# Kernel tuning notes

Measured on AMD Instinct MI355X. Metric: run time of the kernel, lower is better.

Reference implementation:

```python
import jax, jax.numpy as jnp
import numpy as np

B, S, D, H, DH = 2, 1024, 1024, 16, 64  # batch, seq, dim_model, heads, dim_head


def setup_inputs() -> dict:
    key = jax.random.key(0)
    ks = jax.random.split(key, 9)
    def W(k):
        return jax.random.normal(k, (D, D), jnp.float32) * 0.02
    z = jnp.zeros((D,), jnp.float32)
    return {
        "x": jax.random.normal(ks[0], (B, S, D), jnp.float32),
        "rel_pos_emb": jax.random.normal(ks[1], (B, S, D), jnp.float32),
        "padding_mask": jnp.zeros((B, S), jnp.int32),
        "Wq": W(ks[2]), "bq": z,
        "Wk": W(ks[3]), "bk": z,
        "Wv": W(ks[4]), "bv": z,
        "Wqr": W(ks[5]), "bqr": z,
        "Wkr": W(ks[6]), "bkr": z,
        "Wc": W(ks[7]), "bc": z,
    }


def reference(x, rel_pos_emb, padding_mask, Wq, bq, Wk, bk, Wv, bv, Wqr, bqr, Wkr, bkr, Wc, bc):
    b, s, d = x.shape

    def proj(t, W_, b_):  # (b,s,D) -> (b,H,s,DH)
        return (t @ W_.T + b_).reshape(b, s, H, DH).transpose(0, 2, 1, 3)

    q = proj(x, Wq, bq)
    k = proj(x, Wk, bk)
    v = proj(x, Wv, bv)
    qr = proj(rel_pos_emb, Wqr, bqr)
    kr = proj(rel_pos_emb, Wkr, bkr)

    # relative position index: clamp(i - j + MAX_REL_POS/2, 0, MAX_REL_POS-1), MAX_REL_POS = S
    idx = jnp.arange(s)
    pos = jnp.clip(idx[:, None] - idx[None, :] + s // 2, 0, s - 1)  # (s,s) int
    pos_b = jnp.broadcast_to(pos[None, None], (b, H, s, s))

    c2c = jnp.einsum('bhid,bhjd->bhij', q, k)
    c2p_att = jnp.einsum('bhid,bhjd->bhij', q, kr)
    c2p = jnp.take_along_axis(c2p_att, pos_b, axis=-1)   # gather along last dim
    p2c_att = jnp.einsum('bhid,bhjd->bhij', qr, k)
    p2c = jnp.take_along_axis(p2c_att, pos_b, axis=-2)   # gather along query dim

    scale = jnp.sqrt(jnp.asarray(3 * DH, jnp.float32))
    scores = (c2c + c2p + p2c) / scale
    scores = jnp.where(padding_mask[:, None, None, :] == 1, -jnp.inf, scores)
    attn = jax.nn.softmax(scores, axis=-1)  # dropout is identity in eval

    out = jnp.einsum('bhij,bhjd->bhid', attn, v)
    out = out.transpose(0, 2, 1, 3).reshape(b, s, H * DH)
    return out @ Wc.T + bc
```

## Files before the change

kernel.cpp:

```cpp
#include <hip/hip_runtime.h>

typedef unsigned short u16;
typedef unsigned int   u32;
typedef __bf16 bf16x8 __attribute__((ext_vector_type(8)));
typedef float  f32x4  __attribute__((ext_vector_type(4)));

__device__ __forceinline__ float b2f(u16 s) { return __uint_as_float(((u32)s) << 16); }
__device__ __forceinline__ u16 f2b(float f) {
  u32 x = __float_as_uint(f);
  return (u16)((x + 0x7FFFu + ((x >> 16) & 1u)) >> 16);
}

#if __has_builtin(__builtin_amdgcn_exp2f)
#define EXP2(x) __builtin_amdgcn_exp2f(x)
#else
#define EXP2(x) exp2f(x)
#endif

template <int C>
__device__ __forceinline__ u32 dppu(u32 s) {
  return (u32)__builtin_amdgcn_update_dpp((int)s, (int)s, C, 0xF, 0xF, false);
}
__device__ __forceinline__ float red_sum16(float x) {
  x += __uint_as_float(dppu<0x128>(__float_as_uint(x)));
  x += __uint_as_float(dppu<0x124>(__float_as_uint(x)));
  x += __uint_as_float(dppu<0x122>(__float_as_uint(x)));
  x += __uint_as_float(dppu<0x121>(__float_as_uint(x)));
  return x;
}

union U16x8 { uint4 u; u16 s[8]; };

__device__ __forceinline__ uint4 cvt8(const float4 a, const float4 b) {
  U16x8 r;
  r.s[0] = f2b(a.x); r.s[1] = f2b(a.y); r.s[2] = f2b(a.z); r.s[3] = f2b(a.w);
  r.s[4] = f2b(b.x); r.s[5] = f2b(b.y); r.s[6] = f2b(b.z); r.s[7] = f2b(b.w);
  return r.u;
}

typedef __attribute__((address_space(3))) u32 lds_u32;
typedef const __attribute__((address_space(1))) u32 glb_u32;
__device__ __forceinline__ void gld16(const u16* gp, u16* lp) {
  __builtin_amdgcn_global_load_lds((glb_u32*)gp, (lds_u32*)lp, 16, 0, 0);
}

struct CvtArgs { const float* s[8]; u16* d[8]; int n[8]; };

__global__ __launch_bounds__(256) void cvt_bf16(CvtArgs c) {
  const int t = blockIdx.y;
  const int i = (blockIdx.x * 256 + threadIdx.x) * 8;
  if (i >= c.n[t]) return;
  const float4 a = *(const float4*)(c.s[t] + i);
  const float4 b = *(const float4*)(c.s[t] + i + 4);
  *(uint4*)(c.d[t] + i) = cvt8(a, b);
}

struct GemmBArgs { const u16* A[5]; const u16* W[5]; const float* Bi[5]; void* C[5]; int vtz; };

template <int BM, int BN, bool OUT_F32>
__global__ __launch_bounds__(256) void gemm_lds(GemmBArgs g, int M, int N, int K) {
  const int z = blockIdx.z;
  const u16* __restrict__ A = g.A[z];
  const u16* __restrict__ W = g.W[z];
  const float* __restrict__ Bi = g.Bi[z];

  const int m0 = blockIdx.y * BM, n0 = blockIdx.x * BN;
  const int tid = threadIdx.x, wv = tid >> 6, lane = tid & 63;
  const int wm = wv >> 1, wn = wv & 1;
  const int lr = lane & 15, lq = lane >> 4;
  constexpr int MT = BM / 32;
  constexpr int NT = BN / 32;

  __shared__ u16 As[BM * 64];
  __shared__ u16 Ws[BN * 64];

  const f32x4 vzero = {0.f, 0.f, 0.f, 0.f};
  f32x4 acc[MT][NT];
#pragma unroll
  for (int i = 0; i < MT; ++i)
#pragma unroll
    for (int j = 0; j < NT; ++j) acc[i][j] = vzero;

  const int srow = lane >> 3;
  const int sc   = (lane & 7) ^ srow;

  for (int kb = 0; kb < K; kb += 64) {
    __syncthreads();
#pragma unroll
    for (int t = 0; t < MT; ++t) {
      const u16* gp = A + (size_t)(m0 + t * 32 + wv * 8 + srow) * K + kb + sc * 8;
      gld16(gp, As + (t * 32 + wv * 8) * 64 + lane * 8);
    }
#pragma unroll
    for (int t = 0; t < NT; ++t) {
      const u16* gp = W + (size_t)(n0 + t * 32 + wv * 8 + srow) * K + kb + sc * 8;
      gld16(gp, Ws + (t * 32 + wv * 8) * 64 + lane * 8);
    }
    __syncthreads();
#pragma unroll
    for (int kk = 0; kk < 2; ++kk) {
      bf16x8 af[MT], bw[NT];
#pragma unroll
      for (int mt = 0; mt < MT; ++mt) {
        const int row = wm * (BM / 2) + mt * 16 + lr;
        af[mt] = *(const bf16x8*)&As[row * 64 + (((kk << 2) | lq) ^ (row & 7)) * 8];
      }
#pragma unroll
      for (int nt = 0; nt < NT; ++nt) {
        const int row = wn * (BN / 2) + nt * 16 + lr;
        bw[nt] = *(const bf16x8*)&Ws[row * 64 + (((kk << 2) | lq) ^ (row & 7)) * 8];
      }
#pragma unroll
      for (int mt = 0; mt < MT; ++mt)
#pragma unroll
        for (int nt = 0; nt < NT; ++nt)
          acc[mt][nt] = __builtin_amdgcn_mfma_f32_16x16x32_bf16(af[mt], bw[nt], acc[mt][nt], 0, 0, 0);
    }
  }

#pragma unroll
  for (int mt = 0; mt < MT; ++mt) {
#pragma unroll
    for (int nt = 0; nt < NT; ++nt) {
      const int col = n0 + wn * (BN / 2) + nt * 16 + lr;
      const float bia = Bi[col];
      const int row0 = m0 + wm * (BM / 2) + mt * 16 + lq * 4;
      if (OUT_F32) {
#pragma unroll
        for (int r = 0; r < 4; ++r)
          ((float*)g.C[z])[(size_t)(row0 + r) * N + col] = acc[mt][nt][r] + bia;
      } else if (z == g.vtz) {
        ushort4 pk;
        pk.x = f2b(acc[mt][nt][0] + bia); pk.y = f2b(acc[mt][nt][1] + bia);
        pk.z = f2b(acc[mt][nt][2] + bia); pk.w = f2b(acc[mt][nt][3] + bia);
        const int bb = row0 >> 10, s0 = row0 & 1023;
        *(ushort4*)((u16*)g.C[z] + ((size_t)bb << 20) + ((size_t)col << 10) + s0) = pk;
      } else {
#pragma unroll
        for (int r = 0; r < 4; ++r)
          ((u16*)g.C[z])[(size_t)(row0 + r) * N + col] = f2b(acc[mt][nt][r] + bia);
      }
    }
  }
}

struct GemmArgs { const void* A[5]; const float* W[5]; const float* Bi[5]; void* C[5]; int vtz; };

template <bool A_F32, bool OUT_F32>
__global__ __launch_bounds__(256) void gemm5(GemmArgs g, int M, int N, int K) {
  const int z = blockIdx.z;
  const float* __restrict__ Wf = g.W[z];
  const float* __restrict__ Bi = g.Bi[z];

  const int m0 = blockIdx.y * 128, n0 = blockIdx.x * 128;
  const int tid = threadIdx.x;
  const int wv = tid >> 6, lane = tid & 63;
  const int wm = wv >> 1, wn = wv & 1;
  const int lr = lane & 15, lq = lane >> 4;

  __shared__ alignas(16) u16 As[128][64];
  __shared__ alignas(16) u16 Ws[128][64];

  const f32x4 vzero = {0.f, 0.f, 0.f, 0.f};
  f32x4 acc[4][4];
#pragma unroll
  for (int i = 0; i < 4; ++i)
#pragma unroll
    for (int j = 0; j < 4; ++j) acc[i][j] = vzero;

  const int srow = tid >> 1;
  const int sc0  = (tid & 1) * 32;
  const float* pw = Wf + (size_t)(n0 + srow) * K + sc0;
  const float* paf = A_F32 ? ((const float*)g.A[z] + (size_t)(m0 + srow) * K + sc0) : nullptr;
  const u16*   pab = A_F32 ? nullptr : ((const u16*)g.A[z] + (size_t)(m0 + srow) * K + sc0);

  for (int k0 = 0; k0 < K; k0 += 64) {
#pragma unroll
    for (int u_ = 0; u_ < 4; ++u_) {
      const float4 w0 = *(const float4*)(pw + k0 + u_ * 8);
      const float4 w1 = *(const float4*)(pw + k0 + u_ * 8 + 4);
      *(uint4*)&Ws[srow][sc0 + u_ * 8] = cvt8(w0, w1);
      if (A_F32) {
        const float4 a0 = *(const float4*)(paf + k0 + u_ * 8);
        const float4 a1 = *(const float4*)(paf + k0 + u_ * 8 + 4);
        *(uint4*)&As[srow][sc0 + u_ * 8] = cvt8(a0, a1);
      } else {
        *(uint4*)&As[srow][sc0 + u_ * 8] = *(const uint4*)(pab + k0 + u_ * 8);
      }
    }
    __syncthreads();
#pragma unroll
    for (int kk = 0; kk < 2; ++kk) {
      bf16x8 af[4], bfr[4];
#pragma unroll
      for (int mt = 0; mt < 4; ++mt)
        af[mt] = *(const bf16x8*)&As[wm * 64 + mt * 16 + lr][kk * 32 + lq * 8];
#pragma unroll
      for (int nt = 0; nt < 4; ++nt)
        bfr[nt] = *(const bf16x8*)&Ws[wn * 64 + nt * 16 + lr][kk * 32 + lq * 8];
#pragma unroll
      for (int mt = 0; mt < 4; ++mt)
#pragma unroll
        for (int nt = 0; nt < 4; ++nt)
          acc[mt][nt] = __builtin_amdgcn_mfma_f32_16x16x32_bf16(af[mt], bfr[nt], acc[mt][nt], 0, 0, 0);
    }
    __syncthreads();
  }

#pragma unroll
  for (int mt = 0; mt < 4; ++mt) {
#pragma unroll
    for (int nt = 0; nt < 4; ++nt) {
      const int col = n0 + wn * 64 + nt * 16 + lr;
      const float bia = Bi[col];
      const int row0 = m0 + wm * 64 + mt * 16 + lq * 4;
      if (OUT_F32) {
#pragma unroll
        for (int r = 0; r < 4; ++r)
          ((float*)g.C[z])[(size_t)(row0 + r) * N + col] = acc[mt][nt][r] + bia;
      } else if (z == g.vtz) {
        ushort4 pk;
        pk.x = f2b(acc[mt][nt][0] + bia); pk.y = f2b(acc[mt][nt][1] + bia);
        pk.z = f2b(acc[mt][nt][2] + bia); pk.w = f2b(acc[mt][nt][3] + bia);
        const int bb = row0 >> 10, s0 = row0 & 1023;
        *(ushort4*)((u16*)g.C[z] + ((size_t)bb << 20) + ((size_t)col << 10) + s0) = pk;
      } else {
#pragma unroll
        for (int r = 0; r < 4; ++r)
          ((u16*)g.C[z])[(size_t)(row0 + r) * N + col] = f2b(acc[mt][nt][r] + bia);
      }
    }
  }
}

__global__ __launch_bounds__(256, 2) void attn_wave(
    const u16* __restrict__ q, const u16* __restrict__ k,
    const u16* __restrict__ vT, const u16* __restrict__ qr,
    const u16* __restrict__ kr, const int* __restrict__ pmask,
    u16* __restrict__ ao) {
  constexpr int S = 1024, Dm = 1024;
  constexpr int GP = 37;
  constexpr int PBP = 74;
  constexpr int WLDS = 9472;

  __shared__ alignas(16) char smem[4 * WLDS];

  const int bx = blockIdx.x;
  const int bh = bx & 31, it = bx >> 5;
  const int bb = bh >> 4, h = bh & 15;
  const int i0 = it * 32;

  const int tid = threadIdx.x;
  const int wv = tid >> 6, lane = tid & 63;
  const int lq = lane >> 4, lr = lane & 15;

  char* wbase = smem + wv * WLDS;
  float* G1f = (float*)wbase;
  float* G2f = (float*)(wbase + 4736);
  u16*   Pb  = (u16*)wbase;

  const u16* qb  = q  + ((size_t)bb << 20) + h * 64;
  const u16* kb  = k  + ((size_t)bb << 20) + h * 64;
  const u16* qrb = qr + ((size_t)bb << 20) + h * 64;
  const u16* krb = kr + ((size_t)bb << 20) + h * 64;
  const u16* vtb = vT + ((size_t)bb << 20) + ((size_t)h << 16);
  const int* pmb = pmask + ((size_t)bb << 10);

  const float kscale = 1.44269504088896f / 13.856406460551018f;

  bf16x8 qf[2][2];
#pragma unroll
  for (int mt = 0; mt < 2; ++mt)
#pragma unroll
    for (int kk = 0; kk < 2; ++kk)
      qf[mt][kk] = *(const bf16x8*)(qb + (size_t)(i0 + mt * 16 + lr) * Dm + kk * 32 + lq * 8);

  const f32x4 vzero = {0.f, 0.f, 0.f, 0.f};
  f32x4 o[2][4];
#pragma unroll
  for (int mt = 0; mt < 2; ++mt)
#pragma unroll
    for (int nd = 0; nd < 4; ++nd) o[mt][nd] = vzero;
  float lst[2][4];
#pragma unroll
  for (int mt = 0; mt < 2; ++mt)
#pragma unroll
    for (int r = 0; r < 4; ++r) lst[mt][r] = 0.f;

#pragma unroll 1
  for (int t8 = 0; t8 < 8; ++t8) {
    const int j0 = (wv + t8 * 4) * 32;
    const int pb_ = i0 - j0 + 481;

    bf16x8 kf[2][2];
#pragma unroll
    for (int nt = 0; nt < 2; ++nt) {
      const u16* kp = kb + (size_t)(j0 + nt * 16 + lr) * Dm + lq * 8;
      kf[nt][0] = *(const bf16x8*)kp;
      kf[nt][1] = *(const bf16x8*)(kp + 32);
    }
    const int mv0 = pmb[j0 + lr], mv1 = pmb[j0 + 16 + lr];

    f32x4 cc[2][2];
#pragma unroll
    for (int mt = 0; mt < 2; ++mt)
#pragma unroll
      for (int nt = 0; nt < 2; ++nt) {
        f32x4 a = vzero;
        a = __builtin_amdgcn_mfma_f32_16x16x32_bf16(qf[mt][0], kf[nt][0], a, 0, 0, 0);
        a = __builtin_amdgcn_mfma_f32_16x16x32_bf16(qf[mt][1], kf[nt][1], a, 0, 0, 0);
        cc[mt][nt] = a;
      }

#pragma unroll
    for (int n4 = 0; n4 < 4; ++n4) {
      int p = pb_ + n4 * 16 + lr;
      p = p < 0 ? 0 : (p > 1023 ? 1023 : p);
      const u16* kp = krb + (size_t)p * Dm + lq * 8;
      const u16* qp = qrb + (size_t)p * Dm + lq * 8;
      const bf16x8 kr0 = *(const bf16x8*)kp;
      const bf16x8 kr1 = *(const bf16x8*)(kp + 32);
      const bf16x8 qr0 = *(const bf16x8*)qp;
      const bf16x8 qr1 = *(const bf16x8*)(qp + 32);
      const int tb = n4 * 16 + lr;
#pragma unroll
      for (int mt = 0; mt < 2; ++mt) {
        f32x4 a = vzero;
        a = __builtin_amdgcn_mfma_f32_16x16x32_bf16(qf[mt][0], kr0, a, 0, 0, 0);
        a = __builtin_amdgcn_mfma_f32_16x16x32_bf16(qf[mt][1], kr1, a, 0, 0, 0);
#pragma unroll
        for (int r = 0; r < 4; ++r) {
          const int arow = mt * 16 + lq * 4 + r;
          int u = tb - arow;
          u = u < -2 ? -2 : (u > 34 ? 34 : u);
          G1f[2 + arow * GP + u] = a[r];
        }
      }
#pragma unroll
      for (int mt = 0; mt < 2; ++mt) {
        f32x4 g = vzero;
        g = __builtin_amdgcn_mfma_f32_16x16x32_bf16(kf[mt][0], qr0, g, 0, 0, 0);
        g = __builtin_amdgcn_mfma_f32_16x16x32_bf16(kf[mt][1], qr1, g, 0, 0, 0);
#pragma unroll
        for (int r = 0; r < 4; ++r) {
          const int brow = mt * 16 + lq * 4 + r;
          int u = tb + brow - 31;
          u = u < -2 ? -2 : (u > 34 ? 34 : u);
          G2f[2 + brow * GP + u] = g[r];
        }
      }
    }

    u32 pk[2][4];
#pragma unroll
    for (int mt = 0; mt < 2; ++mt) {
#pragma unroll
      for (int r = 0; r < 4; ++r) {
        const int a_ = mt * 16 + lq * 4 + r;
        float s0 = cc[mt][0][r] + G1f[2 + a_ * GP + 31 - lr] + G2f[2 + lr * GP + a_];
        float s1 = cc[mt][1][r] + G1f[2 + a_ * GP + 15 - lr] + G2f[2 + (16 + lr) * GP + a_];
        s0 = mv0 ? -1e30f : s0 * kscale;
        s1 = mv1 ? -1e30f : s1 * kscale;
        const float p0 = EXP2(s0);
        const float p1 = EXP2(s1);
        lst[mt][r] += p0 + p1;
        pk[mt][r] = (u32)f2b(p0) | ((u32)f2b(p1) << 16);
      }
    }
    __asm__ volatile("" ::: "memory");
#pragma unroll
    for (int mt = 0; mt < 2; ++mt)
#pragma unroll
      for (int r = 0; r < 4; ++r) {
        const int a_ = mt * 16 + lq * 4 + r;
        Pb[a_ * PBP + lr]      = (u16)pk[mt][r];
        Pb[a_ * PBP + 16 + lr] = (u16)(pk[mt][r] >> 16);
      }

    bf16x8 vf[4];
#pragma unroll
    for (int n4 = 0; n4 < 4; ++n4)
      vf[n4] = *(const bf16x8*)(vtb + (size_t)(n4 * 16 + lr) * S + j0 + lq * 8);

#pragma unroll
    for (int mt = 0; mt < 2; ++mt) {
      union { u32 u[4]; bf16x8 v; } pr;
      const u16* prow = Pb + (mt * 16 + lr) * PBP + lq * 8;
      pr.u[0] = *(const u32*)prow;
      pr.u[1] = *(const u32*)(prow + 2);
      pr.u[2] = *(const u32*)(prow + 4);
      pr.u[3] = *(const u32*)(prow + 6);
#pragma unroll
      for (int nd = 0; nd < 4; ++nd)
        o[mt][nd] = __builtin_amdgcn_mfma_f32_16x16x32_bf16(pr.v, vf[nd], o[mt][nd], 0, 0, 0);
    }
    __asm__ volatile("" ::: "memory");
  }

  {
    float* Orm = (float*)wbase;
    float* llw = (float*)(wbase + 8192);
#pragma unroll
    for (int mt = 0; mt < 2; ++mt)
#pragma unroll
      for (int nd = 0; nd < 4; ++nd)
#pragma unroll
        for (int r = 0; r < 4; ++r)
          Orm[(mt * 16 + lq * 4 + r) * 64 + nd * 16 + lr] = o[mt][nd][r];
#pragma unroll
    for (int mt = 0; mt < 2; ++mt)
#pragma unroll
      for (int r = 0; r < 4; ++r) {
        const float rl = red_sum16(lst[mt][r]);
        if (lr == 0) llw[mt * 16 + lq * 4 + r] = rl;
      }
  }
  __syncthreads();
  {
    const int a_ = tid >> 3, d0 = (tid & 7) * 8;
    float L = 0.f, acc[8];
#pragma unroll
    for (int d = 0; d < 8; ++d) acc[d] = 0.f;
#pragma unroll
    for (int w = 0; w < 4; ++w) {
      const char* wb = smem + w * WLDS;
      L += *(const float*)(wb + 8192 + a_ * 4);
      const float* Ow = (const float*)wb + a_ * 64 + d0;
#pragma unroll
      for (int d = 0; d < 8; ++d) acc[d] += Ow[d];
    }
    const float inv = 1.f / L;
    U16x8 pk;
#pragma unroll
    for (int d = 0; d < 8; ++d) pk.s[d] = f2b(acc[d] * inv);
    *(uint4*)(ao + ((size_t)((bb << 10) + i0 + a_) << 10) + (h << 6) + d0) = pk.u;
  }
}

extern "C" void kernel_launch(void* const* d_in, const int* in_sizes, int n_in,
                              void* d_out, int out_size, void* d_ws, size_t ws_size,
                              hipStream_t stream) {
  const float* x   = (const float*)d_in[0];
  const float* rpe = (const float*)d_in[1];
  const int*   pm  = (const int*)d_in[2];
  const float* Wq  = (const float*)d_in[3];  const float* bq  = (const float*)d_in[4];
  const float* Wk  = (const float*)d_in[5];  const float* bk  = (const float*)d_in[6];
  const float* Wv  = (const float*)d_in[7];  const float* bv  = (const float*)d_in[8];
  const float* Wqr = (const float*)d_in[9];  const float* bqr = (const float*)d_in[10];
  const float* Wkr = (const float*)d_in[11]; const float* bkr = (const float*)d_in[12];
  const float* Wc  = (const float*)d_in[13]; const float* bc  = (const float*)d_in[14];

  const size_t NE = (size_t)2 * 1024 * 1024;
  const size_t WE = (size_t)1024 * 1024;
  u16* ws = (u16*)d_ws;

  if (ws_size >= (10 * NE + 6 * WE) * sizeof(u16)) {
    u16* q   = ws;          u16* k   = ws + NE;     u16* vT  = ws + 2 * NE;
    u16* qr  = ws + 3 * NE; u16* kr  = ws + 4 * NE;
    u16* xb  = ws + 5 * NE;
    u16* ao  = ws + 5 * NE;
    u16* rpb = ws + 6 * NE;
    u16* wb  = ws + 7 * NE;
    u16* Wqb = wb;           u16* Wkb = wb + WE;     u16* Wvb = wb + 2 * WE;
    u16* Wqrb= wb + 3 * WE;  u16* Wkrb= wb + 4 * WE; u16* Wcb = wb + 5 * WE;

    CvtArgs c;
    c.s[0] = x;   c.d[0] = xb;   c.n[0] = (int)NE;
    c.s[1] = rpe; c.d[1] = rpb;  c.n[1] = (int)NE;
    c.s[2] = Wq;  c.d[2] = Wqb;  c.n[2] = (int)WE;
    c.s[3] = Wk;  c.d[3] = Wkb;  c.n[3] = (int)WE;
    c.s[4] = Wv;  c.d[4] = Wvb;  c.n[4] = (int)WE;
    c.s[5] = Wqr; c.d[5] = Wqrb; c.n[5] = (int)WE;
    c.s[6] = Wkr; c.d[6] = Wkrb; c.n[6] = (int)WE;
    c.s[7] = Wc;  c.d[7] = Wcb;  c.n[7] = (int)WE;
    cvt_bf16<<<dim3(1024, 8), 256, 0, stream>>>(c);

    GemmBArgs g;
    g.A[0] = xb;  g.W[0] = Wqb;  g.Bi[0] = bq;  g.C[0] = q;
    g.A[1] = xb;  g.W[1] = Wkb;  g.Bi[1] = bk;  g.C[1] = k;
    g.A[2] = xb;  g.W[2] = Wvb;  g.Bi[2] = bv;  g.C[2] = vT;
    g.A[3] = rpb; g.W[3] = Wqrb; g.Bi[3] = bqr; g.C[3] = qr;
    g.A[4] = rpb; g.W[4] = Wkrb; g.Bi[4] = bkr; g.C[4] = kr;
    g.vtz = 2;
    gemm_lds<128, 128, false><<<dim3(8, 16, 5), 256, 0, stream>>>(g, 2048, 1024, 1024);

    attn_wave<<<dim3(1024), 256, 0, stream>>>(q, k, vT, qr, kr, pm, ao);

    GemmBArgs g2;
    for (int i = 0; i < 5; ++i) { g2.A[i] = ao; g2.W[i] = Wcb; g2.Bi[i] = bc; g2.C[i] = d_out; }
    g2.vtz = -1;
    gemm_lds<64, 64, true><<<dim3(16, 32, 1), 256, 0, stream>>>(g2, 2048, 1024, 1024);
  } else {
    if (ws_size < 6 * NE * sizeof(u16)) return;
    u16* q  = ws;          u16* k  = ws + NE;     u16* vT = ws + 2 * NE;
    u16* qr = ws + 3 * NE; u16* kr = ws + 4 * NE; u16* ao = ws + 5 * NE;

    GemmArgs g;
    g.A[0] = x;   g.W[0] = Wq;  g.Bi[0] = bq;  g.C[0] = q;
    g.A[1] = x;   g.W[1] = Wk;  g.Bi[1] = bk;  g.C[1] = k;
    g.A[2] = x;   g.W[2] = Wv;  g.Bi[2] = bv;  g.C[2] = vT;
    g.A[3] = rpe; g.W[3] = Wqr; g.Bi[3] = bqr; g.C[3] = qr;
    g.A[4] = rpe; g.W[4] = Wkr; g.Bi[4] = bkr; g.C[4] = kr;
    g.vtz = 2;
    gemm5<true, false><<<dim3(8, 16, 5), 256, 0, stream>>>(g, 2048, 1024, 1024);

    attn_wave<<<dim3(1024), 256, 0, stream>>>(q, k, vT, qr, kr, pm, ao);

    GemmArgs g2;
    for (int i = 0; i < 5; ++i) { g2.A[i] = ao; g2.W[i] = Wc; g2.Bi[i] = bc; g2.C[i] = d_out; }
    g2.vtz = -1;
    gemm5<false, true><<<dim3(8, 16, 1), 256, 0, stream>>>(g2, 2048, 1024, 1024);
  }
}
```

Baseline: 232.3 us.

## Widen attention key tile to 64 per wave and store c2p band in bf16

Each wave now processes 64 keys per iteration instead of 32, so the loop runs 4 times instead of 8. The relative-position band is computed with 6 slices of 16 instead of 4, which cuts the redundant kr/qr loads and MFMAs for overlapping diagonals per key. The c2p band is stored in LDS as bf16 to save space. LDS per wave grows from 9472 to 15360 bytes and register pressure rises, which can lower occupancy. The bf16 rounding of c2p scores adds precision loss.

```diff
diff --git a/kernel.cpp b/kernel.cpp
--- a/kernel.cpp
+++ b/kernel.cpp
@@ -239,9 +239,10 @@
     const u16* __restrict__ kr, const int* __restrict__ pmask,
     u16* __restrict__ ao) {
   constexpr int S = 1024, Dm = 1024;
-  constexpr int GP = 37;
-  constexpr int PBP = 74;
-  constexpr int WLDS = 9472;
+  constexpr int G1P = 76;
+  constexpr int G2P = 41;
+  constexpr int PBP = 76;
+  constexpr int WLDS = 15360;
 
   __shared__ alignas(16) char smem[4 * WLDS];
 
@@ -255,8 +256,8 @@
   const int lq = lane >> 4, lr = lane & 15;
 
   char* wbase = smem + wv * WLDS;
-  float* G1f = (float*)wbase;
-  float* G2f = (float*)(wbase + 4736);
+  u16*   G1b = (u16*)wbase;
+  float* G2f = (float*)(wbase + 4864);
   u16*   Pb  = (u16*)wbase;
 
   const u16* qb  = q  + ((size_t)bb << 20) + h * 64;
@@ -288,24 +289,26 @@
     for (int r = 0; r < 4; ++r) lst[mt][r] = 0.f;
 
 #pragma unroll 1
-  for (int t8 = 0; t8 < 8; ++t8) {
-    const int j0 = (wv + t8 * 4) * 32;
-    const int pb_ = i0 - j0 + 481;
-
-    bf16x8 kf[2][2];
-#pragma unroll
-    for (int nt = 0; nt < 2; ++nt) {
+  for (int t4 = 0; t4 < 4; ++t4) {
+    const int j0 = (wv + t4 * 4) * 64;
+    const int pb_ = i0 - j0 + 449;
+
+    bf16x8 kf[4][2];
+#pragma unroll
+    for (int nt = 0; nt < 4; ++nt) {
       const u16* kp = kb + (size_t)(j0 + nt * 16 + lr) * Dm + lq * 8;
       kf[nt][0] = *(const bf16x8*)kp;
       kf[nt][1] = *(const bf16x8*)(kp + 32);
     }
-    const int mv0 = pmb[j0 + lr], mv1 = pmb[j0 + 16 + lr];
-
-    f32x4 cc[2][2];
+    int mv[4];
+#pragma unroll
+    for (int nt = 0; nt < 4; ++nt) mv[nt] = pmb[j0 + nt * 16 + lr];
+
+    f32x4 cc[2][4];
 #pragma unroll
     for (int mt = 0; mt < 2; ++mt)
 #pragma unroll
-      for (int nt = 0; nt < 2; ++nt) {
+      for (int nt = 0; nt < 4; ++nt) {
         f32x4 a = vzero;
         a = __builtin_amdgcn_mfma_f32_16x16x32_bf16(qf[mt][0], kf[nt][0], a, 0, 0, 0);
         a = __builtin_amdgcn_mfma_f32_16x16x32_bf16(qf[mt][1], kf[nt][1], a, 0, 0, 0);
@@ -313,8 +316,8 @@
       }
 
 #pragma unroll
-    for (int n4 = 0; n4 < 4; ++n4) {
-      int p = pb_ + n4 * 16 + lr;
+    for (int sl = 0; sl < 6; ++sl) {
+      int p = pb_ + sl * 16 + lr;
       p = p < 0 ? 0 : (p > 1023 ? 1023 : p);
       const u16* kp = krb + (size_t)p * Dm + lq * 8;
       const u16* qp = qrb + (size_t)p * Dm + lq * 8;
@@ -322,7 +325,7 @@
       const bf16x8 kr1 = *(const bf16x8*)(kp + 32);
       const bf16x8 qr0 = *(const bf16x8*)qp;
       const bf16x8 qr1 = *(const bf16x8*)(qp + 32);
-      const int tb = n4 * 16 + lr;
+      const int tb = sl * 16 + lr;
 #pragma unroll
       for (int mt = 0; mt < 2; ++mt) {
         f32x4 a = vzero;
@@ -332,39 +335,43 @@
         for (int r = 0; r < 4; ++r) {
           const int arow = mt * 16 + lq * 4 + r;
           int u = tb - arow;
-          u = u < -2 ? -2 : (u > 34 ? 34 : u);
-          G1f[2 + arow * GP + u] = a[r];
+          u = u < -2 ? -2 : (u > 66 ? 66 : u);
+          G1b[arow * G1P + 2 + u] = f2b(a[r]);
         }
       }
 #pragma unroll
-      for (int mt = 0; mt < 2; ++mt) {
+      for (int mt = 0; mt < 4; ++mt) {
         f32x4 g = vzero;
         g = __builtin_amdgcn_mfma_f32_16x16x32_bf16(kf[mt][0], qr0, g, 0, 0, 0);
         g = __builtin_amdgcn_mfma_f32_16x16x32_bf16(kf[mt][1], qr1, g, 0, 0, 0);
 #pragma unroll
         for (int r = 0; r < 4; ++r) {
           const int brow = mt * 16 + lq * 4 + r;
-          int u = tb + brow - 31;
+          int u = tb + brow - 63;
           u = u < -2 ? -2 : (u > 34 ? 34 : u);
-          G2f[2 + brow * GP + u] = g[r];
+          G2f[brow * G2P + 2 + u] = g[r];
         }
       }
     }
 
-    u32 pk[2][4];
+    u32 pk[2][4][2];
 #pragma unroll
     for (int mt = 0; mt < 2; ++mt) {
 #pragma unroll
       for (int r = 0; r < 4; ++r) {
         const int a_ = mt * 16 + lq * 4 + r;
-        float s0 = cc[mt][0][r] + G1f[2 + a_ * GP + 31 - lr] + G2f[2 + lr * GP + a_];
-        float s1 = cc[mt][1][r] + G1f[2 + a_ * GP + 15 - lr] + G2f[2 + (16 + lr) * GP + a_];
-        s0 = mv0 ? -1e30f : s0 * kscale;
-        s1 = mv1 ? -1e30f : s1 * kscale;
-        const float p0 = EXP2(s0);
-        const float p1 = EXP2(s1);
-        lst[mt][r] += p0 + p1;
-        pk[mt][r] = (u32)f2b(p0) | ((u32)f2b(p1) << 16);
+        float p4[4];
+#pragma unroll
+        for (int nt = 0; nt < 4; ++nt) {
+          const int bl = nt * 16 + lr;
+          float s = cc[mt][nt][r] + b2f(G1b[a_ * G1P + 65 - bl]) + G2f[bl * G2P + 2 + a_];
+          s = mv[nt] ? -1e30f : s * kscale;
+          const float p = EXP2(s);
+          lst[mt][r] += p;
+          p4[nt] = p;
+        }
+        pk[mt][r][0] = (u32)f2b(p4[0]) | ((u32)f2b(p4[1]) << 16);
+        pk[mt][r][1] = (u32)f2b(p4[2]) | ((u32)f2b(p4[3]) << 16);
       }
     }
     __asm__ volatile("" ::: "memory");
@@ -373,26 +380,35 @@
 #pragma unroll
       for (int r = 0; r < 4; ++r) {
         const int a_ = mt * 16 + lq * 4 + r;
-        Pb[a_ * PBP + lr]      = (u16)pk[mt][r];
-        Pb[a_ * PBP + 16 + lr] = (u16)(pk[mt][r] >> 16);
-      }
-
-    bf16x8 vf[4];
-#pragma unroll
-    for (int n4 = 0; n4 < 4; ++n4)
-      vf[n4] = *(const bf16x8*)(vtb + (size_t)(n4 * 16 + lr) * S + j0 + lq * 8);
+        Pb[a_ * PBP + lr]      = (u16)pk[mt][r][0];
+        Pb[a_ * PBP + 16 + lr] = (u16)(pk[mt][r][0] >> 16);
+        Pb[a_ * PBP + 32 + lr] = (u16)pk[mt][r][1];
+        Pb[a_ * PBP + 48 + lr] = (u16)(pk[mt][r][1] >> 16);
+      }
+
+    bf16x8 vf[4][2];
+#pragma unroll
+    for (int nd = 0; nd < 4; ++nd)
+#pragma unroll
+      for (int kk = 0; kk < 2; ++kk)
+        vf[nd][kk] = *(const bf16x8*)(vtb + (size_t)(nd * 16 + lr) * S + j0 + kk * 32 + lq * 8);
 
 #pragma unroll
     for (int mt = 0; mt < 2; ++mt) {
-      union { u32 u[4]; bf16x8 v; } pr;
-      const u16* prow = Pb + (mt * 16 + lr) * PBP + lq * 8;
-      pr.u[0] = *(const u32*)prow;
-      pr.u[1] = *(const u32*)(prow + 2);
-      pr.u[2] = *(const u32*)(prow + 4);
-      pr.u[3] = *(const u32*)(prow + 6);
-#pragma unroll
-      for (int nd = 0; nd < 4; ++nd)
-        o[mt][nd] = __builtin_amdgcn_mfma_f32_16x16x32_bf16(pr.v, vf[nd], o[mt][nd], 0, 0, 0);
+      union { u32 u[4]; bf16x8 v; } pr[2];
+#pragma unroll
+      for (int kk = 0; kk < 2; ++kk) {
+        const u16* prow = Pb + (mt * 16 + lr) * PBP + kk * 32 + lq * 8;
+        pr[kk].u[0] = *(const u32*)prow;
+        pr[kk].u[1] = *(const u32*)(prow + 2);
+        pr[kk].u[2] = *(const u32*)(prow + 4);
+        pr[kk].u[3] = *(const u32*)(prow + 6);
+      }
+#pragma unroll
+      for (int nd = 0; nd < 4; ++nd) {
+        o[mt][nd] = __builtin_amdgcn_mfma_f32_16x16x32_bf16(pr[0].v, vf[nd][0], o[mt][nd], 0, 0, 0);
+        o[mt][nd] = __builtin_amdgcn_mfma_f32_16x16x32_bf16(pr[1].v, vf[nd][1], o[mt][nd], 0, 0, 0);
+      }
     }
     __asm__ volatile("" ::: "memory");
   }
```

New measurement: 332.2 us. 1.43x slower.
